# Kernel tuning notes

Hardware: AMD Instinct MI355X
Metric: run time of the kernel (lower is better)

The kernel has to match this reference:

```python
import jax, jax.numpy as jnp
import numpy as np

N_NODES = 40000
N_EDGES = 320000
N_GRAPHS = 64
IN_DIM = 128
HID4 = 256   # hidden_dim * 4
OUT_DIM = 128
LN_EPS = 1e-5


def setup_inputs() -> dict:
    key = jax.random.key(0)
    ks = jax.random.split(key, 12)
    x = jax.random.normal(ks[0], (N_NODES, IN_DIM), dtype=jnp.float32)
    w = jax.random.uniform(ks[1], (N_EDGES, 4), dtype=jnp.float32)
    src = jax.random.randint(ks[2], (N_EDGES,), 0, N_NODES, dtype=jnp.int32)
    dst = jax.random.randint(ks[3], (N_EDGES,), 0, N_NODES, dtype=jnp.int32)
    graph_ids = jnp.sort(jax.random.randint(ks[4], (N_NODES,), 0, N_GRAPHS, dtype=jnp.int32))
    # parameters (no biases on GraphConv / fc1 linear)
    W1 = jax.random.normal(ks[5], (IN_DIM, HID4), dtype=jnp.float32) / np.sqrt(IN_DIM)
    fc1_W = jax.random.normal(ks[6], (IN_DIM, HID4), dtype=jnp.float32) / np.sqrt(IN_DIM)
    ln_gamma = jnp.ones((HID4,), dtype=jnp.float32)
    ln_beta = jnp.zeros((HID4,), dtype=jnp.float32)
    W2 = jax.random.normal(ks[7], (2 * HID4, HID4), dtype=jnp.float32) / np.sqrt(2 * HID4)
    W3 = jax.random.normal(ks[8], (HID4, OUT_DIM), dtype=jnp.float32) / np.sqrt(HID4)
    return {"x": x, "w": w, "W1": W1, "fc1_W": fc1_W, "ln_gamma": ln_gamma,
            "ln_beta": ln_beta, "W2": W2, "W3": W3,
            "src": src, "dst": dst, "graph_ids": graph_ids}


def _graph_conv(feat, src, dst, ew, W, out_inv_sqrt, in_inv_sqrt):
    # DGL GraphConv, norm='both', bias=False, with scalar edge_weight:
    # h = D_out^{-1/2} x ; m_e = w_e * h[src] ; agg = scatter_add(m, dst) ;
    # out = (D_in^{-1/2} agg) @ W
    h = feat * out_inv_sqrt[:, None]
    m = h[src] * ew[:, None]                       # [E, D] messages
    agg = jax.ops.segment_sum(m, dst, num_segments=N_NODES)
    return (agg * in_inv_sqrt[:, None]) @ W


def reference(x, w, W1, fc1_W, ln_gamma, ln_beta, W2, W3, src, dst, graph_ids):
    # unweighted degree normalization (DGL uses structural degrees, clamp(min=1))
    ones_e = jnp.ones((N_EDGES,), dtype=x.dtype)
    out_deg = jnp.maximum(jax.ops.segment_sum(ones_e, src, num_segments=N_NODES), 1.0)
    in_deg = jnp.maximum(jax.ops.segment_sum(ones_e, dst, num_segments=N_NODES), 1.0)
    out_inv = out_deg ** -0.5
    in_inv = in_deg ** -0.5

    ew = jnp.max(w, axis=1)                        # [E]

    x1 = jax.nn.relu(_graph_conv(x, src, dst, ew, W1, out_inv, in_inv))

    # fc1: Linear(no bias) -> LayerNorm(affine) -> ReLU
    f1 = x @ fc1_W
    mu = jnp.mean(f1, axis=-1, keepdims=True)
    var = jnp.mean((f1 - mu) ** 2, axis=-1, keepdims=True)
    f1 = (f1 - mu) * jax.lax.rsqrt(var + LN_EPS) * ln_gamma + ln_beta
    f1 = jax.nn.relu(f1)

    x1f1 = jnp.concatenate([x1, f1], axis=1)       # [N, 512]
    x2 = jax.nn.relu(_graph_conv(x1f1, src, dst, ew, W2, out_inv, in_inv))
    x3 = jax.nn.relu(_graph_conv(x2, src, dst, ew, W3, out_inv, in_inv))

    # dgl.sum_nodes over batched graph, then row-wise L2 normalize
    readout = jax.ops.segment_sum(x3, graph_ids, num_segments=N_GRAPHS)  # [G, OUT_DIM]
    norm = jnp.maximum(jnp.linalg.norm(readout, axis=1, keepdims=True), 1e-12)
    return readout / norm
```

## Files before the change

### kernel.cpp

```cpp
#include <hip/hip_runtime.h>

#define N_NODES 40000
#define M_PAD   40064
#define N_EDGES 320000
#define N_GRAPHS 64
#define IN_DIM 128
#define HID4 256
#define OUT_DIM 128
#define LN_EPS 1e-5f

typedef short  s16x8  __attribute__((ext_vector_type(8)));
typedef __bf16 bf16x8 __attribute__((ext_vector_type(8)));
typedef float  f32x4  __attribute__((ext_vector_type(4)));

__device__ __forceinline__ unsigned short f2b(float f) {
    unsigned int u = __builtin_bit_cast(unsigned int, f);
    u += 0x7fffu + ((u >> 16) & 1u);
    return (unsigned short)(u >> 16);
}
__device__ __forceinline__ float b2f(unsigned short h) {
    unsigned int u = (unsigned int)h << 16;
    return __builtin_bit_cast(float, u);
}
__device__ __forceinline__ float lo2f(unsigned int u) { return b2f((unsigned short)u); }
__device__ __forceinline__ float hi2f(unsigned int u) { return b2f((unsigned short)(u >> 16)); }
__device__ __forceinline__ unsigned int packb(float x, float y) {
    return (unsigned int)f2b(x) | ((unsigned int)f2b(y) << 16);
}

__device__ __forceinline__ void gll16(const unsigned short* g, short* lds_base) {
    __builtin_amdgcn_global_load_lds(
        (const __attribute__((address_space(1))) unsigned int*)g,
        (__attribute__((address_space(3))) unsigned int*)lds_base, 16, 0, 0);
}


#define XN (N_NODES * IN_DIM)
#define WN 229376
#define PREP_TOT (XN + WN + N_EDGES)

__global__ void prep_all(const float* __restrict__ x, const float* __restrict__ W1,
                         const float* __restrict__ fc1, const float* __restrict__ W2,
                         const float* __restrict__ W3, const float* __restrict__ w,
                         const int* __restrict__ src, const int* __restrict__ dst,
                         unsigned short* __restrict__ xb, unsigned short* __restrict__ W1t,
                         unsigned short* __restrict__ fc1t, unsigned short* __restrict__ W2t,
                         unsigned short* __restrict__ W3t, float* __restrict__ ew,
                         int* __restrict__ cnt_out, int* __restrict__ cnt_in) {
    int idx = blockIdx.x * 256 + threadIdx.x;
    if (idx < XN) { xb[idx] = f2b(x[idx]); return; }
    int j = idx - XN;
    if (j < 32768) { int k = j >> 8, n = j & 255; W1t[n * 128 + k] = f2b(W1[j]); return; }
    j -= 32768;
    if (j < 32768) { int k = j >> 8, n = j & 255; fc1t[n * 128 + k] = f2b(fc1[j]); return; }
    j -= 32768;
    if (j < 131072) { int k = j >> 8, n = j & 255; W2t[n * 512 + k] = f2b(W2[j]); return; }
    j -= 131072;
    if (j < 32768) { int k = j >> 7, n = j & 127; W3t[n * 256 + k] = f2b(W3[j]); return; }
    j -= 32768;
    if (j < N_EDGES) {
        float4 v = ((const float4*)w)[j];
        ew[j] = fmaxf(fmaxf(v.x, v.y), fmaxf(v.z, v.w));
        atomicAdd(&cnt_out[src[j]], 1);
        atomicAdd(&cnt_in[dst[j]], 1);
    }
}

__global__ void scan_part(const int* __restrict__ cnt, int* __restrict__ partial) {
    int b = blockIdx.x;
    int s = 0;
    for (int i = threadIdx.x; i < 1000; i += 256) s += cnt[b * 1000 + i];
#pragma unroll
    for (int m = 1; m < 64; m <<= 1) s += __shfl_xor(s, m);
    __shared__ int wsm[4];
    if ((threadIdx.x & 63) == 0) wsm[threadIdx.x >> 6] = s;
    __syncthreads();
    if (threadIdx.x == 0) partial[b] = wsm[0] + wsm[1] + wsm[2] + wsm[3];
}

__global__ void scan_final(const int* __restrict__ cnt_in, const int* __restrict__ cnt_out,
                           const int* __restrict__ partial, int* __restrict__ off,
                           float* __restrict__ out_inv, float* __restrict__ in_inv) {
    int b = blockIdx.x, tid = threadIdx.x;
    int lane = tid & 63, wv = tid >> 6;
    int pre = 0;
    for (int j = 0; j < b; ++j) pre += partial[j];
    int i = b * 1000 + tid;
    int v = (tid < 1000) ? cnt_in[i] : 0;
    int x = v;
#pragma unroll
    for (int ofs = 1; ofs < 64; ofs <<= 1) {
        int t = __shfl_up(x, ofs);
        if (lane >= ofs) x += t;
    }
    __shared__ int wsum[16];
    if (lane == 63) wsum[wv] = x;
    __syncthreads();
    if (wv == 0 && lane < 16) {
        int s = wsum[lane];
#pragma unroll
        for (int ofs = 1; ofs < 16; ofs <<= 1) {
            int t = __shfl_up(s, ofs);
            if (lane >= ofs) s += t;
        }
        wsum[lane] = s;
    }
    __syncthreads();
    int incl = pre + (wv > 0 ? wsum[wv - 1] : 0) + x;
    if (tid < 1000) {
        off[i] = incl - v;
        in_inv[i] = rsqrtf(fmaxf((float)v, 1.0f));
        out_inv[i] = rsqrtf(fmaxf((float)cnt_out[i], 1.0f));
    }
    if (b == 39 && tid == 999) off[N_NODES] = incl;
}

__global__ void csr_fill(const int* __restrict__ src, const int* __restrict__ dst,
                         const float* __restrict__ ew, const float* __restrict__ out_inv,
                         const int* __restrict__ off, int* __restrict__ cnt_in,
                         int4* __restrict__ es) {
    int e = blockIdx.x * 256 + threadIdx.x;
    if (e >= N_EDGES) return;
    int d = dst[e];
    int slot = off[d] + atomicSub(&cnt_in[d], 1) - 1;
    int s = src[e];
    float wv = ew[e];
    es[slot] = make_int4(s, __float_as_int(wv * out_inv[s]), __float_as_int(wv), 0);
}


template <int D, int RELU, int WSEL>
__global__ void gather_nodes(const unsigned short* __restrict__ h, const int* __restrict__ off,
                             const int4* __restrict__ eg, const float* __restrict__ scale,
                             unsigned short* __restrict__ outb) {
    int n = blockIdx.x;
    int lane = threadIdx.x;
    int b = off[n], e = off[n + 1];
    const uint2* hu = (const uint2*)h;
    float a0 = 0.f, a1 = 0.f, a2 = 0.f, a3 = 0.f;
    if constexpr (D == 256) {
        int i = b;
        for (; i + 3 < e; i += 4) {
            int4 e0 = eg[i], e1 = eg[i + 1], e2 = eg[i + 2], e3 = eg[i + 3];
            uint2 p0 = hu[(size_t)e0.x * 64 + lane];
            uint2 p1 = hu[(size_t)e1.x * 64 + lane];
            uint2 p2 = hu[(size_t)e2.x * 64 + lane];
            uint2 p3 = hu[(size_t)e3.x * 64 + lane];
            float w0 = __int_as_float(WSEL ? e0.z : e0.y);
            float w1 = __int_as_float(WSEL ? e1.z : e1.y);
            float w2 = __int_as_float(WSEL ? e2.z : e2.y);
            float w3 = __int_as_float(WSEL ? e3.z : e3.y);
            a0 += w0 * lo2f(p0.x) + w1 * lo2f(p1.x) + w2 * lo2f(p2.x) + w3 * lo2f(p3.x);
            a1 += w0 * hi2f(p0.x) + w1 * hi2f(p1.x) + w2 * hi2f(p2.x) + w3 * hi2f(p3.x);
            a2 += w0 * lo2f(p0.y) + w1 * lo2f(p1.y) + w2 * lo2f(p2.y) + w3 * lo2f(p3.y);
            a3 += w0 * hi2f(p0.y) + w1 * hi2f(p1.y) + w2 * hi2f(p2.y) + w3 * hi2f(p3.y);
        }
        for (; i < e; ++i) {
            int4 ee = eg[i];
            uint2 p = hu[(size_t)ee.x * 64 + lane];
            float w0 = __int_as_float(WSEL ? ee.z : ee.y);
            a0 += w0 * lo2f(p.x); a1 += w0 * hi2f(p.x);
            a2 += w0 * lo2f(p.y); a3 += w0 * hi2f(p.y);
        }
        float sc = scale[n];
        a0 *= sc; a1 *= sc; a2 *= sc; a3 *= sc;
        if (RELU) {
            a0 = fmaxf(a0, 0.f); a1 = fmaxf(a1, 0.f);
            a2 = fmaxf(a2, 0.f); a3 = fmaxf(a3, 0.f);
        }
        uint2 o; o.x = packb(a0, a1); o.y = packb(a2, a3);
        ((uint2*)outb)[(size_t)n * 64 + lane] = o;
    } else {
        int half = lane >> 5, cl = lane & 31;
        int i = b;
        for (; i + 3 < e; i += 4) {
            int4 ea = eg[i + half];
            int4 eb = eg[i + 2 + half];
            uint2 pa = hu[(size_t)ea.x * 32 + cl];
            uint2 pb = hu[(size_t)eb.x * 32 + cl];
            float wa = __int_as_float(WSEL ? ea.z : ea.y);
            float wb = __int_as_float(WSEL ? eb.z : eb.y);
            a0 += wa * lo2f(pa.x) + wb * lo2f(pb.x);
            a1 += wa * hi2f(pa.x) + wb * hi2f(pb.x);
            a2 += wa * lo2f(pa.y) + wb * lo2f(pb.y);
            a3 += wa * hi2f(pa.y) + wb * hi2f(pb.y);
        }
        for (; i < e; i += 2) {
            int idx = i + half;
            int4 ee = eg[idx < e ? idx : i];
            float w = (idx < e) ? __int_as_float(WSEL ? ee.z : ee.y) : 0.0f;
            uint2 p = hu[(size_t)ee.x * 32 + cl];
            a0 += w * lo2f(p.x); a1 += w * hi2f(p.x);
            a2 += w * lo2f(p.y); a3 += w * hi2f(p.y);
        }
        a0 += __shfl_xor(a0, 32); a1 += __shfl_xor(a1, 32);
        a2 += __shfl_xor(a2, 32); a3 += __shfl_xor(a3, 32);
        float sc = scale[n];
        a0 *= sc; a1 *= sc; a2 *= sc; a3 *= sc;
        if (RELU) {
            a0 = fmaxf(a0, 0.f); a1 = fmaxf(a1, 0.f);
            a2 = fmaxf(a2, 0.f); a3 = fmaxf(a3, 0.f);
        }
        if (half == 0) {
            uint2 o; o.x = packb(a0, a1); o.y = packb(a2, a3);
            ((uint2*)outb)[(size_t)n * 32 + cl] = o;
        }
    }
}


#define G3_NPB 8

__global__ void gather3_ro(const unsigned short* __restrict__ h, const int* __restrict__ off,
                           const int4* __restrict__ eg, const float* __restrict__ scale,
                           const int* __restrict__ gid, float* __restrict__ ro) {
    int lane = threadIdx.x;
    int half = lane >> 5, cl = lane & 31;
    int n0 = blockIdx.x * G3_NPB;
    int n1 = n0 + G3_NPB;
    if (n1 > N_NODES) n1 = N_NODES;
    const uint2* hu = (const uint2*)h;
    float r0 = 0.f, r1 = 0.f, r2 = 0.f, r3 = 0.f;
    int cur = gid[n0];
    for (int n = n0; n < n1; ++n) {
        int g = gid[n];
        if (g != cur) {
            atomicAdd(&ro[cur * OUT_DIM + 4 * cl + 2 * half], half ? r2 : r0);
            atomicAdd(&ro[cur * OUT_DIM + 4 * cl + 2 * half + 1], half ? r3 : r1);
            r0 = r1 = r2 = r3 = 0.f;
            cur = g;
        }
        int b = off[n], e = off[n + 1];
        float a0 = 0.f, a1 = 0.f, a2 = 0.f, a3 = 0.f;
        int i = b;
        for (; i + 3 < e; i += 4) {
            int4 ea = eg[i + half];
            int4 eb = eg[i + 2 + half];
            uint2 pa = hu[(size_t)ea.x * 32 + cl];
            uint2 pb = hu[(size_t)eb.x * 32 + cl];
            float wa = __int_as_float(ea.z), wb = __int_as_float(eb.z);
            a0 += wa * lo2f(pa.x) + wb * lo2f(pb.x);
            a1 += wa * hi2f(pa.x) + wb * hi2f(pb.x);
            a2 += wa * lo2f(pa.y) + wb * lo2f(pb.y);
            a3 += wa * hi2f(pa.y) + wb * hi2f(pb.y);
        }
        for (; i < e; i += 2) {
            int idx = i + half;
            int4 ee = eg[idx < e ? idx : i];
            float w = (idx < e) ? __int_as_float(ee.z) : 0.0f;
            uint2 p = hu[(size_t)ee.x * 32 + cl];
            a0 += w * lo2f(p.x); a1 += w * hi2f(p.x);
            a2 += w * lo2f(p.y); a3 += w * hi2f(p.y);
        }
        a0 += __shfl_xor(a0, 32); a1 += __shfl_xor(a1, 32);
        a2 += __shfl_xor(a2, 32); a3 += __shfl_xor(a3, 32);
        float sc = scale[n];
        r0 += fmaxf(a0 * sc, 0.0f);
        r1 += fmaxf(a1 * sc, 0.0f);
        r2 += fmaxf(a2 * sc, 0.0f);
        r3 += fmaxf(a3 * sc, 0.0f);
    }
    atomicAdd(&ro[cur * OUT_DIM + 4 * cl + 2 * half], half ? r2 : r0);
    atomicAdd(&ro[cur * OUT_DIM + 4 * cl + 2 * half + 1], half ? r3 : r1);
}


__device__ __forceinline__ void gemm_core(short* As, short* Bs,
    const unsigned short* __restrict__ A, const unsigned short* __restrict__ A2,
    const unsigned short* __restrict__ Bt, unsigned short* __restrict__ C,
    const float* __restrict__ rowScaleC, int K1, int K2, int N,
    int relu, int scaleC, int m0, int n0) {
    int tid = threadIdx.x;
    int lane = tid & 63, wave = tid >> 6;
    int wm = (wave >> 1) * 64, wn = (wave & 1) * 64;
    int quad = lane >> 4, r16 = lane & 15;
    const int K = K1 + K2;
    f32x4 acc[4][4] = {};
    int srow = lane >> 3;
    int sk   = ((lane & 7) ^ srow) * 8;
    int xorc = r16 & 7;
    short* ldsA = As + wave * 2048;
    short* ldsB = Bs + wave * 2048;

    for (int k0 = 0; k0 < K; k0 += 64) {
        int kk = k0 + sk;
#pragma unroll
        for (int h = 0; h < 4; ++h) {
            int r = wave * 32 + h * 8 + srow;
            const unsigned short* Ap = (k0 < K1)
                ? A  + (size_t)(m0 + r) * K1 + kk
                : A2 + (size_t)(m0 + r) * K2 + (kk - K1);
            gll16(Ap, ldsA + h * 512);
            gll16(Bt + (size_t)(n0 + r) * K + kk, ldsB + h * 512);
        }
        __syncthreads();
#pragma unroll
        for (int c = 0; c < 2; ++c) {
            s16x8 af[4], bfr[4];
            int pc = (((c * 4 + quad) ^ xorc) << 3);
#pragma unroll
            for (int i = 0; i < 4; ++i)
                af[i] = *(const s16x8*)(As + (wm + i * 16 + r16) * 64 + pc);
#pragma unroll
            for (int j = 0; j < 4; ++j)
                bfr[j] = *(const s16x8*)(Bs + (wn + j * 16 + r16) * 64 + pc);
#pragma unroll
            for (int i = 0; i < 4; ++i)
#pragma unroll
                for (int j = 0; j < 4; ++j)
                    acc[i][j] = __builtin_amdgcn_mfma_f32_16x16x32_bf16(
                        __builtin_bit_cast(bf16x8, af[i]), __builtin_bit_cast(bf16x8, bfr[j]),
                        acc[i][j], 0, 0, 0);
        }
        __syncthreads();
    }

#pragma unroll
    for (int i = 0; i < 4; ++i) {
        int mbase = m0 + wm + i * 16 + quad * 4;
#pragma unroll
        for (int r = 0; r < 4; ++r) {
            int m = mbase + r;
            float sc = scaleC ? rowScaleC[m] : 1.0f;
#pragma unroll
            for (int j = 0; j < 4; ++j) {
                float v = acc[i][j][r] * sc;
                if (relu) v = fmaxf(v, 0.0f);
                C[(size_t)m * N + n0 + wn + j * 16 + r16] = f2b(v);
            }
        }
    }
}

template <int RELU, int SCALE_C>
__global__ __launch_bounds__(256) void gemm_mfma(
    const unsigned short* __restrict__ A, const unsigned short* __restrict__ A2,
    const unsigned short* __restrict__ Bt, unsigned short* __restrict__ C,
    const float* __restrict__ rowScaleC, int K1, int K2, int N) {
    __shared__ short As[8192];
    __shared__ short Bs[8192];
    gemm_core(As, Bs, A, A2, Bt, C, rowScaleC, K1, K2, N, RELU, SCALE_C,
              blockIdx.x * 128, blockIdx.y * 128);
}


__global__ __launch_bounds__(512) void gemm_dual(
    const unsigned short* __restrict__ A0, const unsigned short* __restrict__ B0,
    unsigned short* __restrict__ C0,
    const unsigned short* __restrict__ A1, const unsigned short* __restrict__ B1,
    unsigned short* __restrict__ C1,
    const float* __restrict__ gamma, const float* __restrict__ beta) {
    __shared__ short As[4096];
    __shared__ short Bs[8192];
    __shared__ float lns[128][4];
    __shared__ float lnq[128][4];
    const unsigned short* A  = blockIdx.z ? A1 : A0;
    const unsigned short* Bt = blockIdx.z ? B1 : B0;
    unsigned short* C        = blockIdx.z ? C1 : C0;
    int tid = threadIdx.x;
    int lane = tid & 63, wave = tid >> 6;
    int wm = (wave >> 2) * 64, wn = (wave & 3) * 64;
    int quad = lane >> 4, r16 = lane & 15;
    int m0 = blockIdx.x * 128;
    f32x4 acc[4][4] = {};
    int lrow = lane >> 2;
    int kc = (lane & 3) * 8;
    short* ldsA = As + wave * 512;
    short* ldsB = Bs + wave * 512;

    for (int k0 = 0; k0 < 128; k0 += 32) {
        int kk = k0 + kc;
        int rr = wave * 16 + lrow;
        gll16(A + (size_t)(m0 + rr) * 128 + kk, ldsA);
        gll16(Bt + (size_t)rr * 128 + kk, ldsB);
        gll16(Bt + (size_t)(128 + rr) * 128 + kk, ldsB + 4096);
        __syncthreads();
        s16x8 af[4], bfr[4];
#pragma unroll
        for (int i = 0; i < 4; ++i)
            af[i] = *(const s16x8*)(As + (wm + i * 16 + r16) * 32 + quad * 8);
#pragma unroll
        for (int j = 0; j < 4; ++j)
            bfr[j] = *(const s16x8*)(Bs + (wn + j * 16 + r16) * 32 + quad * 8);
#pragma unroll
        for (int i = 0; i < 4; ++i)
#pragma unroll
            for (int j = 0; j < 4; ++j)
                acc[i][j] = __builtin_amdgcn_mfma_f32_16x16x32_bf16(
                    __builtin_bit_cast(bf16x8, af[i]), __builtin_bit_cast(bf16x8, bfr[j]),
                    acc[i][j], 0, 0, 0);
        __syncthreads();
    }

    if (blockIdx.z == 0) {
#pragma unroll
        for (int i = 0; i < 4; ++i) {
            int mbase = m0 + wm + i * 16 + quad * 4;
#pragma unroll
            for (int r = 0; r < 4; ++r) {
                int m = mbase + r;
#pragma unroll
                for (int j = 0; j < 4; ++j)
                    C[(size_t)m * 256 + wn + j * 16 + r16] = f2b(fmaxf(acc[i][j][r], 0.0f));
            }
        }
    } else {
#pragma unroll
        for (int i = 0; i < 4; ++i)
#pragma unroll
            for (int r = 0; r < 4; ++r) {
                float s = 0.0f, q = 0.0f;
#pragma unroll
                for (int j = 0; j < 4; ++j) { float v = acc[i][j][r]; s += v; q += v * v; }
#pragma unroll
                for (int m = 1; m < 16; m <<= 1) { s += __shfl_xor(s, m); q += __shfl_xor(q, m); }
                if (r16 == 0) {
                    int row = wm + i * 16 + quad * 4 + r;
                    lns[row][wave & 3] = s;
                    lnq[row][wave & 3] = q;
                }
            }
        __syncthreads();
#pragma unroll
        for (int i = 0; i < 4; ++i) {
#pragma unroll
            for (int r = 0; r < 4; ++r) {
                int row = wm + i * 16 + quad * 4 + r;
                float s = lns[row][0] + lns[row][1] + lns[row][2] + lns[row][3];
                float q = lnq[row][0] + lnq[row][1] + lnq[row][2] + lnq[row][3];
                float mu = s * (1.0f / HID4);
                float var = q * (1.0f / HID4) - mu * mu;
                float rs = rsqrtf(var + LN_EPS);
                int m = m0 + row;
#pragma unroll
                for (int j = 0; j < 4; ++j) {
                    int col = wn + j * 16 + r16;
                    float v = (acc[i][j][r] - mu) * rs * gamma[col] + beta[col];
                    C[(size_t)m * 256 + col] = f2b(fmaxf(v, 0.0f));
                }
            }
        }
    }
}


__global__ void normalize_out(const float* __restrict__ ro, float* __restrict__ out) {
    int g = blockIdx.x;
    int d = threadIdx.x;
    float v = ro[g * OUT_DIM + d];
    float ss = v * v;
#pragma unroll
    for (int m = 1; m < 64; m <<= 1) ss += __shfl_xor(ss, m);
    __shared__ float s2[2];
    if ((d & 63) == 0) s2[d >> 6] = ss;
    __syncthreads();
    float tot = s2[0] + s2[1];
    float norm = fmaxf(sqrtf(tot), 1e-12f);
    out[g * OUT_DIM + d] = v / norm;
}


extern "C" void kernel_launch(void* const* d_in, const int* in_sizes, int n_in,
                              void* d_out, int out_size, void* d_ws, size_t ws_size,
                              hipStream_t stream) {
    const float* x    = (const float*)d_in[0];
    const float* w    = (const float*)d_in[1];
    const float* W1   = (const float*)d_in[2];
    const float* fc1W = (const float*)d_in[3];
    const float* gam  = (const float*)d_in[4];
    const float* bet  = (const float*)d_in[5];
    const float* W2   = (const float*)d_in[6];
    const float* W3   = (const float*)d_in[7];
    const int* src = (const int*)d_in[8];
    const int* dst = (const int*)d_in[9];
    const int* gid = (const int*)d_in[10];
    float* out = (float*)d_out;

    float* ws = (float*)d_ws;
    float* out_inv = ws + 0;
    float* in_inv  = ws + 40000;
    float* ew      = ws + 80000;
    int*   cnt_out = (int*)(ws + 400000);
    int*   cnt_in  = (int*)(ws + 440000);
    float* ro      = ws + 480000;
    unsigned short* W1t  = (unsigned short*)(ws + 488192);
    unsigned short* fc1t = (unsigned short*)(ws + 504576);
    unsigned short* W2t  = (unsigned short*)(ws + 520960);
    unsigned short* W3t  = (unsigned short*)(ws + 586496);
    int*   partial = (int*)(ws + 602880);
    int*   off     = (int*)(ws + 602920);
    int4*  es      = (int4*)(ws + 642924);
    unsigned short* xb    = (unsigned short*)(ws + 1923000);
    unsigned short* Q3b   = xb;
    unsigned short* agg1b = (unsigned short*)(ws + 4487100);
    unsigned short* x2b   = agg1b;
    unsigned short* x1b   = (unsigned short*)(ws + 9615300);
    unsigned short* f1b   = (unsigned short*)(ws + 14743500);
    unsigned short* P2b   = (unsigned short*)(ws + 19871700);

    hipMemsetAsync(cnt_out, 0, (2 * 40000 + N_GRAPHS * OUT_DIM) * sizeof(float), stream);

    prep_all<<<(PREP_TOT + 255) / 256, 256, 0, stream>>>(x, W1, fc1W, W2, W3, w, src, dst,
                                                         xb, W1t, fc1t, W2t, W3t, ew,
                                                         cnt_out, cnt_in);
    scan_part<<<40, 256, 0, stream>>>(cnt_in, partial);
    scan_final<<<40, 1024, 0, stream>>>(cnt_in, cnt_out, partial, off, out_inv, in_inv);
    csr_fill<<<(N_EDGES + 255) / 256, 256, 0, stream>>>(src, dst, ew, out_inv, off, cnt_in, es);

    gather_nodes<IN_DIM, 0, 0><<<N_NODES, 64, 0, stream>>>(xb, off, es, in_inv, agg1b);
    {
        dim3 grid(M_PAD / 128, 1, 2);
        gemm_dual<<<grid, 512, 0, stream>>>(agg1b, W1t, x1b, xb, fc1t, f1b, gam, bet);
    }

    {
        dim3 grid(M_PAD / 128, HID4 / 128);
        gemm_mfma<0, 1><<<grid, 256, 0, stream>>>(x1b, f1b, W2t, P2b, out_inv,
                                                  HID4, HID4, HID4);
    }
    gather_nodes<HID4, 1, 1><<<N_NODES, 64, 0, stream>>>(P2b, off, es, in_inv, x2b);

    {
        dim3 grid(M_PAD / 128, OUT_DIM / 128);
        gemm_mfma<0, 1><<<grid, 256, 0, stream>>>(x2b, nullptr, W3t, Q3b, out_inv,
                                                  HID4, 0, OUT_DIM);
    }
    gather3_ro<<<(N_NODES + G3_NPB - 1) / G3_NPB, 64, 0, stream>>>(Q3b, off, es, in_inv,
                                                                   gid, ro);
    normalize_out<<<N_GRAPHS, 128, 0, stream>>>(ro, out);
}
```

Baseline: 285.0 us.

## Fuse scan kernels, overlap CSR fill with fc1 GEMM, fold normalize into readout

Merges the two-pass prefix scan into a single kernel in which each block recomputes its own prefix sum. Runs the CSR fill and the fc1+LayerNorm GEMM in one launch as separate block ranges, and splits the conv1 GEMM off on its own. Folds the final L2 normalization into the last block of gather3_ro using a completion counter. The x bf16 conversion now handles eight elements per thread. Together these remove several launches and let independent work overlap, at the cost of redundant scan reads and a serial tail in the last readout block.

Result: slower. 428.3 us (+50.3%).

```diff
diff --git a/kernel.cpp b/kernel.cpp
--- a/kernel.cpp
+++ b/kernel.cpp
@@ -34,10 +34,14 @@
         (__attribute__((address_space(3))) unsigned int*)lds_base, 16, 0, 0);
 }
 
+#define MFMA_BF16(a, b, c) __builtin_amdgcn_mfma_f32_16x16x32_bf16( \
+    __builtin_bit_cast(bf16x8, a), __builtin_bit_cast(bf16x8, b), c, 0, 0, 0)
+
 
 #define XN (N_NODES * IN_DIM)
+#define XT (XN / 8)
 #define WN 229376
-#define PREP_TOT (XN + WN + N_EDGES)
+#define PREP_TOT (XT + WN + N_EDGES)
 
 __global__ void prep_all(const float* __restrict__ x, const float* __restrict__ W1,
                          const float* __restrict__ fc1, const float* __restrict__ W2,
@@ -46,10 +50,20 @@
                          unsigned short* __restrict__ xb, unsigned short* __restrict__ W1t,
                          unsigned short* __restrict__ fc1t, unsigned short* __restrict__ W2t,
                          unsigned short* __restrict__ W3t, float* __restrict__ ew,
-                         int* __restrict__ cnt_out, int* __restrict__ cnt_in) {
+                         int* __restrict__ cnt_out, int* __restrict__ cnt_in,
+                         int* __restrict__ done) {
     int idx = blockIdx.x * 256 + threadIdx.x;
-    if (idx < XN) { xb[idx] = f2b(x[idx]); return; }
-    int j = idx - XN;
+    if (idx == 0) *done = 0;
+    if (idx < XT) {
+        const float4* xv = (const float4*)x;
+        float4 u = xv[idx * 2], v = xv[idx * 2 + 1];
+        uint4 o;
+        o.x = packb(u.x, u.y); o.y = packb(u.z, u.w);
+        o.z = packb(v.x, v.y); o.w = packb(v.z, v.w);
+        ((uint4*)xb)[idx] = o;
+        return;
+    }
+    int j = idx - XT;
     if (j < 32768) { int k = j >> 8, n = j & 255; W1t[n * 128 + k] = f2b(W1[j]); return; }
     j -= 32768;
     if (j < 32768) { int k = j >> 8, n = j & 255; fc1t[n * 128 + k] = f2b(fc1[j]); return; }
@@ -66,25 +80,22 @@
     }
 }
 
-__global__ void scan_part(const int* __restrict__ cnt, int* __restrict__ partial) {
-    int b = blockIdx.x;
-    int s = 0;
-    for (int i = threadIdx.x; i < 1000; i += 256) s += cnt[b * 1000 + i];
-#pragma unroll
-    for (int m = 1; m < 64; m <<= 1) s += __shfl_xor(s, m);
-    __shared__ int wsm[4];
-    if ((threadIdx.x & 63) == 0) wsm[threadIdx.x >> 6] = s;
-    __syncthreads();
-    if (threadIdx.x == 0) partial[b] = wsm[0] + wsm[1] + wsm[2] + wsm[3];
-}
-
-__global__ void scan_final(const int* __restrict__ cnt_in, const int* __restrict__ cnt_out,
-                           const int* __restrict__ partial, int* __restrict__ off,
-                           float* __restrict__ out_inv, float* __restrict__ in_inv) {
+__global__ __launch_bounds__(1024) void scan_fused(
+        const int* __restrict__ cnt_in, const int* __restrict__ cnt_out,
+        int* __restrict__ off, float* __restrict__ out_inv, float* __restrict__ in_inv) {
     int b = blockIdx.x, tid = threadIdx.x;
     int lane = tid & 63, wv = tid >> 6;
+    int s = 0;
+    for (int i = tid; i < b * 1000; i += 1024) s += cnt_in[i];
+#pragma unroll
+    for (int m = 1; m < 64; m <<= 1) s += __shfl_xor(s, m);
+    __shared__ int wred[16];
+    __shared__ int wsum[16];
+    if (lane == 0) wred[wv] = s;
+    __syncthreads();
     int pre = 0;
-    for (int j = 0; j < b; ++j) pre += partial[j];
+#pragma unroll
+    for (int k = 0; k < 16; ++k) pre += wred[k];
     int i = b * 1000 + tid;
     int v = (tid < 1000) ? cnt_in[i] : 0;
     int x = v;
@@ -93,17 +104,16 @@
         int t = __shfl_up(x, ofs);
         if (lane >= ofs) x += t;
     }
-    __shared__ int wsum[16];
     if (lane == 63) wsum[wv] = x;
     __syncthreads();
     if (wv == 0 && lane < 16) {
-        int s = wsum[lane];
+        int s2 = wsum[lane];
 #pragma unroll
         for (int ofs = 1; ofs < 16; ofs <<= 1) {
-            int t = __shfl_up(s, ofs);
-            if (lane >= ofs) s += t;
-        }
-        wsum[lane] = s;
+            int t = __shfl_up(s2, ofs);
+            if (lane >= ofs) s2 += t;
+        }
+        wsum[lane] = s2;
     }
     __syncthreads();
     int incl = pre + (wv > 0 ? wsum[wv - 1] : 0) + x;
@@ -115,17 +125,96 @@
     if (b == 39 && tid == 999) off[N_NODES] = incl;
 }
 
-__global__ void csr_fill(const int* __restrict__ src, const int* __restrict__ dst,
-                         const float* __restrict__ ew, const float* __restrict__ out_inv,
-                         const int* __restrict__ off, int* __restrict__ cnt_in,
-                         int4* __restrict__ es) {
-    int e = blockIdx.x * 256 + threadIdx.x;
-    if (e >= N_EDGES) return;
-    int d = dst[e];
-    int slot = off[d] + atomicSub(&cnt_in[d], 1) - 1;
-    int s = src[e];
-    float wv = ew[e];
-    es[slot] = make_int4(s, __float_as_int(wv * out_inv[s]), __float_as_int(wv), 0);
+
+__global__ __launch_bounds__(512) void csr_fc1(
+    const int* __restrict__ src, const int* __restrict__ dst,
+    const float* __restrict__ ew, const float* __restrict__ out_inv,
+    const int* __restrict__ off, int* __restrict__ cnt_in, int4* __restrict__ es,
+    const unsigned short* __restrict__ A, const unsigned short* __restrict__ Bt,
+    unsigned short* __restrict__ C,
+    const float* __restrict__ gamma, const float* __restrict__ beta) {
+    __shared__ short As[4096];
+    __shared__ short Bs[8192];
+    __shared__ float lns[128][4];
+    __shared__ float lnq[128][4];
+    if (blockIdx.x < 625) {
+        int e = blockIdx.x * 512 + threadIdx.x;
+        if (e >= N_EDGES) return;
+        int d = dst[e];
+        int slot = off[d] + atomicSub(&cnt_in[d], 1) - 1;
+        int s = src[e];
+        float wv = ew[e];
+        es[slot] = make_int4(s, __float_as_int(wv * out_inv[s]), __float_as_int(wv), 0);
+        return;
+    }
+    int m0 = (blockIdx.x - 625) * 128;
+    int tid = threadIdx.x;
+    int lane = tid & 63, wave = tid >> 6;
+    int wm = (wave >> 2) * 64, wn = (wave & 3) * 64;
+    int quad = lane >> 4, r16 = lane & 15;
+    f32x4 acc[4][4] = {};
+    int lrow = lane >> 2;
+    int kc = (lane & 3) * 8;
+    short* ldsA = As + wave * 512;
+    short* ldsB = Bs + wave * 512;
+
+    for (int k0 = 0; k0 < 128; k0 += 32) {
+        int kk = k0 + kc;
+        int rr = wave * 16 + lrow;
+        gll16(A + (size_t)(m0 + rr) * 128 + kk, ldsA);
+        gll16(Bt + (size_t)rr * 128 + kk, ldsB);
+        gll16(Bt + (size_t)(128 + rr) * 128 + kk, ldsB + 4096);
+        __syncthreads();
+        s16x8 af[4], bfr[4];
+#pragma unroll
+        for (int i = 0; i < 4; ++i)
+            af[i] = *(const s16x8*)(As + (wm + i * 16 + r16) * 32 + quad * 8);
+#pragma unroll
+        for (int j = 0; j < 4; ++j)
+            bfr[j] = *(const s16x8*)(Bs + (wn + j * 16 + r16) * 32 + quad * 8);
+#pragma unroll
+        for (int i = 0; i < 4; ++i)
+#pragma unroll
+            for (int j = 0; j < 4; ++j)
+                acc[i][j] = MFMA_BF16(af[i], bfr[j], acc[i][j]);
+        __syncthreads();
+    }
+
+#pragma unroll
+    for (int i = 0; i < 4; ++i)
+#pragma unroll
+        for (int r = 0; r < 4; ++r) {
+            float s = 0.0f, q = 0.0f;
+#pragma unroll
+            for (int j = 0; j < 4; ++j) { float v = acc[i][j][r]; s += v; q += v * v; }
+#pragma unroll
+            for (int m = 1; m < 16; m <<= 1) { s += __shfl_xor(s, m); q += __shfl_xor(q, m); }
+            if (r16 == 0) {
+                int row = wm + i * 16 + quad * 4 + r;
+                lns[row][wave & 3] = s;
+                lnq[row][wave & 3] = q;
+            }
+        }
+    __syncthreads();
+#pragma unroll
+    for (int i = 0; i < 4; ++i) {
+#pragma unroll
+        for (int r = 0; r < 4; ++r) {
+            int row = wm + i * 16 + quad * 4 + r;
+            float s = lns[row][0] + lns[row][1] + lns[row][2] + lns[row][3];
+            float q = lnq[row][0] + lnq[row][1] + lnq[row][2] + lnq[row][3];
+            float mu = s * (1.0f / HID4);
+            float var = q * (1.0f / HID4) - mu * mu;
+            float rs = rsqrtf(var + LN_EPS);
+            int m = m0 + row;
+#pragma unroll
+            for (int j = 0; j < 4; ++j) {
+                int col = wn + j * 16 + r16;
+                float v = (acc[i][j][r] - mu) * rs * gamma[col] + beta[col];
+                C[(size_t)m * 256 + col] = f2b(fmaxf(v, 0.0f));
+            }
+        }
+    }
 }
 
 
@@ -213,7 +302,8 @@
 
 __global__ void gather3_ro(const unsigned short* __restrict__ h, const int* __restrict__ off,
                            const int4* __restrict__ eg, const float* __restrict__ scale,
-                           const int* __restrict__ gid, float* __restrict__ ro) {
+                           const int* __restrict__ gid, float* __restrict__ ro,
+                           float* __restrict__ out, int* __restrict__ done) {
     int lane = threadIdx.x;
     int half = lane >> 5, cl = lane & 31;
     int n0 = blockIdx.x * G3_NPB;
@@ -255,13 +345,34 @@
         a0 += __shfl_xor(a0, 32); a1 += __shfl_xor(a1, 32);
         a2 += __shfl_xor(a2, 32); a3 += __shfl_xor(a3, 32);
         float sc = scale[n];
-        r0 += fmaxf(a0 * sc, 0.0f);
-        r1 += fmaxf(a1 * sc, 0.0f);
-        r2 += fmaxf(a2 * sc, 0.0f);
-        r3 += fmaxf(a3 * sc, 0.0f);
+        r0 += fmaxf(a0 * sc, 0.0f); r1 += fmaxf(a1 * sc, 0.0f);
+        r2 += fmaxf(a2 * sc, 0.0f); r3 += fmaxf(a3 * sc, 0.0f);
     }
     atomicAdd(&ro[cur * OUT_DIM + 4 * cl + 2 * half], half ? r2 : r0);
     atomicAdd(&ro[cur * OUT_DIM + 4 * cl + 2 * half + 1], half ? r3 : r1);
+
+    __shared__ int islast;
+    if (lane == 0) {
+        __threadfence();
+        int t = atomicAdd(done, 1);
+        islast = (t == (int)gridDim.x - 1) ? 1 : 0;
+    }
+    __syncthreads();
+    if (islast) {
+        int g = lane;
+        float ss = 0.0f;
+        for (int d = 0; d < OUT_DIM; ++d) {
+            float v = __hip_atomic_load(&ro[g * OUT_DIM + d], __ATOMIC_RELAXED,
+                                        __HIP_MEMORY_SCOPE_AGENT);
+            ss += v * v;
+        }
+        float inv = 1.0f / fmaxf(sqrtf(ss), 1e-12f);
+        for (int d = 0; d < OUT_DIM; ++d) {
+            float v = __hip_atomic_load(&ro[g * OUT_DIM + d], __ATOMIC_RELAXED,
+                                        __HIP_MEMORY_SCOPE_AGENT);
+            out[g * OUT_DIM + d] = v * inv;
+        }
+    }
 }
 
 
@@ -308,9 +419,7 @@
             for (int i = 0; i < 4; ++i)
 #pragma unroll
                 for (int j = 0; j < 4; ++j)
-                    acc[i][j] = __builtin_amdgcn_mfma_f32_16x16x32_bf16(
-                        __builtin_bit_cast(bf16x8, af[i]), __builtin_bit_cast(bf16x8, bfr[j]),
-                        acc[i][j], 0, 0, 0);
+                    acc[i][j] = MFMA_BF16(af[i], bfr[j], acc[i][j]);
         }
         __syncthreads();
     }
@@ -344,19 +453,11 @@
 }
 
 
-__global__ __launch_bounds__(512) void gemm_dual(
-    const unsigned short* __restrict__ A0, const unsigned short* __restrict__ B0,
-    unsigned short* __restrict__ C0,
-    const unsigned short* __restrict__ A1, const unsigned short* __restrict__ B1,
-    unsigned short* __restrict__ C1,
-    const float* __restrict__ gamma, const float* __restrict__ beta) {
+__global__ __launch_bounds__(512) void gemm_conv1(
+    const unsigned short* __restrict__ A, const unsigned short* __restrict__ Bt,
+    unsigned short* __restrict__ C) {
     __shared__ short As[4096];
     __shared__ short Bs[8192];
-    __shared__ float lns[128][4];
-    __shared__ float lnq[128][4];
-    const unsigned short* A  = blockIdx.z ? A1 : A0;
-    const unsigned short* Bt = blockIdx.z ? B1 : B0;
-    unsigned short* C        = blockIdx.z ? C1 : C0;
     int tid = threadIdx.x;
     int lane = tid & 63, wave = tid >> 6;
     int wm = (wave >> 2) * 64, wn = (wave & 3) * 64;
@@ -386,77 +487,21 @@
         for (int i = 0; i < 4; ++i)
 #pragma unroll
             for (int j = 0; j < 4; ++j)
-                acc[i][j] = __builtin_amdgcn_mfma_f32_16x16x32_bf16(
-                    __builtin_bit_cast(bf16x8, af[i]), __builtin_bit_cast(bf16x8, bfr[j]),
-                    acc[i][j], 0, 0, 0);
+                acc[i][j] = MFMA_BF16(af[i], bfr[j], acc[i][j]);
         __syncthreads();
     }
 
-    if (blockIdx.z == 0) {
-#pragma unroll
-        for (int i = 0; i < 4; ++i) {
-            int mbase = m0 + wm + i * 16 + quad * 4;
-#pragma unroll
-            for (int r = 0; r < 4; ++r) {
-                int m = mbase + r;
-#pragma unroll
-                for (int j = 0; j < 4; ++j)
-                    C[(size_t)m * 256 + wn + j * 16 + r16] = f2b(fmaxf(acc[i][j][r], 0.0f));
-            }
-        }
-    } else {
-#pragma unroll
-        for (int i = 0; i < 4; ++i)
-#pragma unroll
-            for (int r = 0; r < 4; ++r) {
-                float s = 0.0f, q = 0.0f;
-#pragma unroll
-                for (int j = 0; j < 4; ++j) { float v = acc[i][j][r]; s += v; q += v * v; }
-#pragma unroll
-                for (int m = 1; m < 16; m <<= 1) { s += __shfl_xor(s, m); q += __shfl_xor(q, m); }
-                if (r16 == 0) {
-                    int row = wm + i * 16 + quad * 4 + r;
-                    lns[row][wave & 3] = s;
-                    lnq[row][wave & 3] = q;
-                }
-            }
-        __syncthreads();
-#pragma unroll
-        for (int i = 0; i < 4; ++i) {
-#pragma unroll
-            for (int r = 0; r < 4; ++r) {
-                int row = wm + i * 16 + quad * 4 + r;
-                float s = lns[row][0] + lns[row][1] + lns[row][2] + lns[row][3];
-                float q = lnq[row][0] + lnq[row][1] + lnq[row][2] + lnq[row][3];
-                float mu = s * (1.0f / HID4);
-                float var = q * (1.0f / HID4) - mu * mu;
-                float rs = rsqrtf(var + LN_EPS);
-                int m = m0 + row;
-#pragma unroll
-                for (int j = 0; j < 4; ++j) {
-                    int col = wn + j * 16 + r16;
-                    float v = (acc[i][j][r] - mu) * rs * gamma[col] + beta[col];
-                    C[(size_t)m * 256 + col] = f2b(fmaxf(v, 0.0f));
-                }
-            }
-        }
-    }
-}
-
-
-__global__ void normalize_out(const float* __restrict__ ro, float* __restrict__ out) {
-    int g = blockIdx.x;
-    int d = threadIdx.x;
-    float v = ro[g * OUT_DIM + d];
-    float ss = v * v;
-#pragma unroll
-    for (int m = 1; m < 64; m <<= 1) ss += __shfl_xor(ss, m);
-    __shared__ float s2[2];
-    if ((d & 63) == 0) s2[d >> 6] = ss;
-    __syncthreads();
-    float tot = s2[0] + s2[1];
-    float norm = fmaxf(sqrtf(tot), 1e-12f);
-    out[g * OUT_DIM + d] = v / norm;
+#pragma unroll
+    for (int i = 0; i < 4; ++i) {
+        int mbase = m0 + wm + i * 16 + quad * 4;
+#pragma unroll
+        for (int r = 0; r < 4; ++r) {
+            int m = mbase + r;
+#pragma unroll
+            for (int j = 0; j < 4; ++j)
+                C[(size_t)m * 256 + wn + j * 16 + r16] = f2b(fmaxf(acc[i][j][r], 0.0f));
+        }
+    }
 }
 
 
@@ -487,7 +532,7 @@
     unsigned short* fc1t = (unsigned short*)(ws + 504576);
     unsigned short* W2t  = (unsigned short*)(ws + 520960);
     unsigned short* W3t  = (unsigned short*)(ws + 586496);
-    int*   partial = (int*)(ws + 602880);
+    int*   done    = (int*)(ws + 602880);
     int*   off     = (int*)(ws + 602920);
     int4*  es      = (int4*)(ws + 642924);
     unsigned short* xb    = (unsigned short*)(ws + 1923000);
@@ -502,16 +547,14 @@
 
     prep_all<<<(PREP_TOT + 255) / 256, 256, 0, stream>>>(x, W1, fc1W, W2, W3, w, src, dst,
                                                          xb, W1t, fc1t, W2t, W3t, ew,
-                                                         cnt_out, cnt_in);
-    scan_part<<<40, 256, 0, stream>>>(cnt_in, partial);
-    scan_final<<<40, 1024, 0, stream>>>(cnt_in, cnt_out, partial, off, out_inv, in_inv);
-    csr_fill<<<(N_EDGES + 255) / 256, 256, 0, stream>>>(src, dst, ew, out_inv, off, cnt_in, es);
+                                                         cnt_out, cnt_in, done);
+    scan_fused<<<40, 1024, 0, stream>>>(cnt_in, cnt_out, off, out_inv, in_inv);
+
+    csr_fc1<<<625 + 313, 512, 0, stream>>>(src, dst, ew, out_inv, off, cnt_in, es,
+                                           xb, fc1t, f1b, gam, bet);
 
     gather_nodes<IN_DIM, 0, 0><<<N_NODES, 64, 0, stream>>>(xb, off, es, in_inv, agg1b);
-    {
-        dim3 grid(M_PAD / 128, 1, 2);
-        gemm_dual<<<grid, 512, 0, stream>>>(agg1b, W1t, x1b, xb, fc1t, f1b, gam, bet);
-    }
+    gemm_conv1<<<313, 512, 0, stream>>>(agg1b, W1t, x1b);
 
     {
         dim3 grid(M_PAD / 128, HID4 / 128);
@@ -526,6 +569,5 @@
                                                   HID4, 0, OUT_DIM);
     }
     gather3_ro<<<(N_NODES + G3_NPB - 1) / G3_NPB, 64, 0, stream>>>(Q3b, off, es, in_inv,
-                                                                   gid, ro);
-    normalize_out<<<N_GRAPHS, 128, 0, stream>>>(ro, out);
-}
+                                                                   gid, ro, out, done);
+}
```
